# Optimization experiments

Measured on AMD Instinct MI355X. Metric: run time of the kernel, lower is better.

## Reference

```python
import math
import jax, jax.numpy as jnp
import numpy as np

B, F, NH, NB = 8, 400, 100, 65
SR, BLOCK = 16000, 128


def scale_function(x):
    # 2 * sigmoid(x)^log(10) + 1e-7 (standard ddsp_pytorch scale_function)
    return 2.0 * jax.nn.sigmoid(x) ** math.log(10.0) + 1e-7


def fft_convolve(signal, kernel):
    # signal: (..., L), kernel: (..., Lk); zero-pad, circular conv via rfft, keep 2nd half
    L = signal.shape[-1]
    Lk = kernel.shape[-1]
    s = jnp.pad(signal, [(0, 0)] * (signal.ndim - 1) + [(0, L)])
    k = jnp.pad(kernel, [(0, 0)] * (kernel.ndim - 1) + [(Lk, 0)])
    out = jnp.fft.irfft(jnp.fft.rfft(s) * jnp.fft.rfft(k))
    return out[..., out.shape[-1] // 2:]


def setup_inputs() -> dict:
    key = jax.random.key(0)
    k1, k2, k3, k4, k5 = jax.random.split(key, 5)
    return {
        "amp_param": jax.random.normal(k1, (B, F, NH + 1), jnp.float32),
        "noise_param": jax.random.normal(k2, (B, F, NB), jnp.float32),
        "pitch": jax.random.uniform(k3, (B, F, 1), jnp.float32) * 440.0 + 60.0,
        "noise": jax.random.uniform(k4, (B, F, BLOCK), jnp.float32) * 2.0 - 1.0,
        "reverb_noise": jax.random.uniform(k5, (SR, 1), jnp.float32) * 2.0 - 1.0,
        "decay": jnp.ones((1,), jnp.float32) * 5.0,
        "wet": jnp.zeros((1,), jnp.float32),
        "sampling_rate": SR,
        "block_size": BLOCK,
    }


def reference(amp_param, noise_param, pitch, noise, reverb_noise, decay, wet,
              sampling_rate, block_size):
    sr = float(sampling_rate)
    # ---- harmonic branch ----
    param = scale_function(amp_param)            # (B,F,NH+1)
    total_amp = param[..., :1]
    amps = param[..., 1:]                        # (B,F,NH)
    nh = amps.shape[-1]
    harm_idx = jnp.arange(1, nh + 1, dtype=amps.dtype)
    # remove_above_nyquist
    aa = (pitch * harm_idx < sr / 2).astype(amps.dtype) + 1e-4
    amps = amps * aa
    amps = amps / amps.sum(-1, keepdims=True)
    amps = amps * total_amp
    # nearest-neighbor upsample by block_size (torch interpolate default 'nearest')
    amps_up = jnp.repeat(amps, block_size, axis=1)    # (B,T,NH)
    pitch_up = jnp.repeat(pitch, block_size, axis=1)  # (B,T,1)
    # harmonic_synth: cumulative phase oscillator bank
    omega = jnp.cumsum(2.0 * math.pi * pitch_up / sr, axis=1)  # (B,T,1)
    harmonic = (jnp.sin(omega * harm_idx) * amps_up).sum(-1, keepdims=True)  # (B,T,1)

    # ---- filtered-noise branch ----
    nparam = scale_function(noise_param - 5.0)   # (B,F,NB)
    ir = jnp.fft.irfft(nparam.astype(jnp.complex64))  # (B,F,2*(NB-1))
    fs = ir.shape[-1]
    ir = jnp.roll(ir, fs // 2, axis=-1)
    win = 0.5 - 0.5 * jnp.cos(2.0 * math.pi * jnp.arange(fs, dtype=ir.dtype) / fs)
    ir = ir * win
    ir = jnp.pad(ir, ((0, 0), (0, 0), (0, block_size - fs)))
    ir = jnp.roll(ir, -(fs // 2), axis=-1)
    nz = fft_convolve(noise, ir)                 # (B,F,block)
    nz = nz.reshape(nz.shape[0], -1, 1)          # (B,T,1)

    signal = harmonic + nz                       # (B,T,1)

    # ---- reverb ----
    lenx = signal.shape[1]
    length = reverb_noise.shape[0]               # == sampling_rate
    t = (jnp.arange(length, dtype=signal.dtype) / sr).reshape(1, -1, 1)
    env = jnp.exp(-jax.nn.softplus(-decay[0]) * t * 500.0)
    impulse = reverb_noise * env * jax.nn.sigmoid(wet[0])   # (1,length,1)
    impulse = impulse.at[:, 0].set(1.0)
    impulse = jnp.pad(impulse, ((0, 0), (0, lenx - length), (0, 0)))
    out = fft_convolve(signal[..., 0], impulse[..., 0])[..., None]  # (B,T,1)
    return out
```

## Files before the change

### kernel.cpp

```cpp
#include <hip/hip_runtime.h>
#include <math.h>

#define NBATCH 8
#define NFRAME 400
#define NHARM  100
#define NBAND  65
#define SRATE  16000
#define BLK    128
#define NSAMP  (NFRAME*BLK)
#define PI_D   3.14159265358979323846

#define FFTN   4096
#define HOP    2048
#define NPART  8
#define NHOPS  (NSAMP / HOP)
#define NPAIR  (NBATCH / 2)
#define FTH    1024
#define NCONV  (NPAIR * NHOPS)

#define OFF_SIG    25600
#define OFF_H      1729536
#define OFF_X      1991680

typedef float2 cplx;

__device__ __forceinline__ int conv_swz(int bid) {
    int xcd = bid & 7, idx = bid >> 3;
    int base = (xcd < 4) ? xcd * 13 : 52 + (xcd - 4) * 12;
    return base + idx;
}

__device__ __forceinline__ cplx cmul(cplx a, cplx b) {
    return make_float2(a.x * b.x - a.y * b.y, a.x * b.y + a.y * b.x);
}
template <int SIGN>
__device__ __forceinline__ cplx rot90(cplx z) {
    return (SIGN < 0) ? make_float2(z.y, -z.x) : make_float2(-z.y, z.x);
}

template <int SIGN>
__device__ __forceinline__ void fft_dif_4096(cplx* A, int tid) {
    #pragma unroll
    for (int t = 12; t >= 2; t -= 2) {
        const int Q = 1 << (t - 2), h = 1 << (t - 1);
        __syncthreads();
        {
            int g = tid;
            int j = g & (Q - 1);
            int a = ((g >> (t - 2)) << t) + j;
            cplx x0 = A[a], x1 = A[a + Q], x2 = A[a + h], x3 = A[a + h + Q];
            float ang = (float)(2.0 * PI_D) * (float)j / (float)(1 << t);
            float sn, cs; __sincosf(ang, &sn, &cs);
            cplx w1 = make_float2(cs, (float)SIGN * sn);
            cplx w3 = make_float2(cs * cs - sn * sn, 2.0f * cs * sn * (float)SIGN);
            cplx p0 = make_float2(x0.x + x2.x, x0.y + x2.y);
            cplx p2 = cmul(make_float2(x0.x - x2.x, x0.y - x2.y), w1);
            cplx p1 = make_float2(x1.x + x3.x, x1.y + x3.y);
            cplx p3 = rot90<SIGN>(cmul(make_float2(x1.x - x3.x, x1.y - x3.y), w1));
            A[a]         = make_float2(p0.x + p1.x, p0.y + p1.y);
            A[a + Q]     = cmul(make_float2(p0.x - p1.x, p0.y - p1.y), w3);
            A[a + h]     = make_float2(p2.x + p3.x, p2.y + p3.y);
            A[a + h + Q] = cmul(make_float2(p2.x - p3.x, p2.y - p3.y), w3);
        }
    }
    __syncthreads();
}

template <int SIGN>
__device__ __forceinline__ void fft_dit_4096(cplx* A, int tid) {
    #pragma unroll
    for (int t = 2; t <= 12; t += 2) {
        const int Q = 1 << (t - 2), h = 1 << (t - 1);
        __syncthreads();
        {
            int g = tid;
            int j = g & (Q - 1);
            int a = ((g >> (t - 2)) << t) + j;
            cplx x0 = A[a], x1 = A[a + Q], x2 = A[a + h], x3 = A[a + h + Q];
            float ang = (float)(2.0 * PI_D) * (float)j / (float)(1 << t);
            float sn, cs; __sincosf(ang, &sn, &cs);
            cplx w1 = make_float2(cs, (float)SIGN * sn);
            cplx w3 = make_float2(cs * cs - sn * sn, 2.0f * cs * sn * (float)SIGN);
            cplx b1 = cmul(x1, w3);
            cplx q0 = make_float2(x0.x + b1.x, x0.y + b1.y);
            cplx q1 = make_float2(x0.x - b1.x, x0.y - b1.y);
            cplx b3 = cmul(x3, w3);
            cplx q2 = make_float2(x2.x + b3.x, x2.y + b3.y);
            cplx q3 = make_float2(x2.x - b3.x, x2.y - b3.y);
            cplx c2 = cmul(q2, w1);
            cplx c3 = rot90<SIGN>(cmul(q3, w1));
            A[a]         = make_float2(q0.x + c2.x, q0.y + c2.y);
            A[a + h]     = make_float2(q0.x - c2.x, q0.y - c2.y);
            A[a + Q]     = make_float2(q1.x + c3.x, q1.y + c3.y);
            A[a + h + Q] = make_float2(q1.x - c3.x, q1.y - c3.y);
        }
    }
    __syncthreads();
}

__device__ __forceinline__ float scale_fn(float x) {
    float s = 1.0f / (1.0f + __expf(-x));
    return 2.0f * __expf(2.3025851f * __logf(s)) + 1e-7f;
}

__global__ __launch_bounds__(128) void k_synth(const float* __restrict__ amp_param,
                                               const float* __restrict__ noise_param,
                                               const float* __restrict__ pitch,
                                               const float* __restrict__ noise,
                                               float* __restrict__ sig) {
    __shared__ float s_famps[NHARM];
    __shared__ float s_np[NBAND];
    __shared__ float s_ir[BLK];
    __shared__ float s_noise[BLK];
    __shared__ float s_red[BLK];
    __shared__ double s_dsum[2];
    __shared__ float s_fsum[2];
    __shared__ float s_total;

    int bf = blockIdx.x;
    int tid = threadIdx.x;
    int b  = bf / NFRAME, f0 = bf % NFRAME;
    float pf = pitch[bf];

    double ps = 0.0;
    {
        const float* prow = pitch + b * NFRAME;
        for (int j = tid; j < f0; j += BLK) ps += (double)prow[j];
    }

    float myamp = 0.0f;
    if (tid < NHARM + 1) {
        float p = scale_fn(amp_param[bf * (NHARM + 1) + tid]);
        if (tid == 0) s_total = p;
        else {
            float aa = (pf * (float)tid < 8000.0f) ? 1.0001f : 0.0001f;
            myamp = p * aa;
        }
    }
    if (tid < NBAND) s_np[tid] = scale_fn(noise_param[bf * NBAND + tid] - 5.0f);
    s_noise[tid] = noise[bf * BLK + tid];

    double rp = ps; float ra = myamp;
    #pragma unroll
    for (int off = 32; off >= 1; off >>= 1) {
        rp += __shfl_xor(rp, off);
        ra += __shfl_xor(ra, off);
    }
    if ((tid & 63) == 0) { s_dsum[tid >> 6] = rp; s_fsum[tid >> 6] = ra; }
    __syncthreads();

    double prefix_b = s_dsum[0] + s_dsum[1];
    float red = s_fsum[0] + s_fsum[1];
    if (tid >= 1 && tid <= NHARM) s_famps[tid - 1] = myamp / red * s_total;

    float irv;
    {
        float ang = (float)(2.0 * PI_D / 128.0) * (float)tid;
        float sn, c; __sincosf(ang, &sn, &c);
        float tcc = 2.0f * c;
        float u1 = c;
        float u2 = fmaf(tcc, u1, -1.0f);
        float u3 = fmaf(tcc, u2, -u1);
        float u4 = fmaf(tcc, u3, -u2);
        float u5 = fmaf(tcc, u4, -u3);
        float u6 = fmaf(tcc, u5, -u4);
        float u7 = fmaf(tcc, u6, -u5);
        float t0 = s_np[4] * u4;
        float t1 = fmaf(s_np[5], u5, s_np[1] * u1);
        float t2 = fmaf(s_np[6], u6, s_np[2] * u2);
        float t3 = fmaf(s_np[7], u7, s_np[3] * u3);
        float cc4  = fmaf(2.0f * u2, u2, -1.0f);
        float tc4a = 2.0f * cc4;
        float A0 = 1.0f, A1 = u1, A2 = u2, A3 = u3;
        float B0 = u4,   B1 = u5, B2 = u6, B3 = u7;
        #pragma unroll
        for (int g = 0; g < 14; ++g) {
            float n0 = fmaf(tc4a, B0, -A0); t0 = fmaf(s_np[8 + 4 * g + 0], n0, t0); A0 = B0; B0 = n0;
            float n1 = fmaf(tc4a, B1, -A1); t1 = fmaf(s_np[8 + 4 * g + 1], n1, t1); A1 = B1; B1 = n1;
            float n2 = fmaf(tc4a, B2, -A2); t2 = fmaf(s_np[8 + 4 * g + 2], n2, t2); A2 = B2; B2 = n2;
            float n3 = fmaf(tc4a, B3, -A3); t3 = fmaf(s_np[8 + 4 * g + 3], n3, t3); A3 = B3; B3 = n3;
        }
        float u64 = fmaf(tc4a, B0, -A0);
        float tt = (t0 + t1) + (t2 + t3);
        float a = fmaf(2.0f, tt, s_np[0]);
        a = fmaf(s_np[64], u64, a);
        a *= (1.0f / 128.0f);
        a *= fmaf(0.5f, c, 0.5f);
        irv = a;
    }
    s_ir[tid] = irv;
    __syncthreads();

    float accA = 0.0f;
    {
        int p1 = tid, h1 = (p1 + 2) >> 1;
        int m = 0;
        for (; m + 1 < h1; m += 2) {
            float i0 = s_ir[p1 - m], i1 = s_ir[p1 - m - 1];
            accA = fmaf(s_noise[m], i0, accA);
            accA = fmaf(s_noise[m + 1], i1, accA);
        }
        if (m < h1) accA = fmaf(s_noise[m], s_ir[p1 - m], accA);
    }
    {
        int p2 = 127 - tid, h2 = (p2 + 2) >> 1;
        float accB = 0.0f;
        int m = h2;
        for (; m + 1 <= p2; m += 2) {
            float i0 = s_ir[p2 - m], i1 = s_ir[p2 - m - 1];
            accB = fmaf(s_noise[m], i0, accB);
            accB = fmaf(s_noise[m + 1], i1, accB);
        }
        if (m <= p2) accB = fmaf(s_noise[m], s_ir[p2 - m], accB);
        s_red[p2] = accB;
    }
    __syncthreads();
    float nzv = accA + s_red[tid];

    double q = (128.0 * prefix_b + (double)(tid + 1) * (double)pf) * (1.0 / 16000.0);
    float th = (float)(q - floor(q)) * (float)(2.0 * PI_D);
    float h;
    {
        float s1v, c1v; __sincosf(th, &s1v, &c1v);
        float tc = 2.0f * c1v;
        float sk0 = s1v;
        float sk1 = tc * s1v;
        float sk2 = fmaf(tc, sk1, -sk0);
        float sk3 = fmaf(tc, sk2, -sk1);
        float sk4 = fmaf(tc, sk3, -sk2);
        float sk5 = fmaf(tc, sk4, -sk3);
        float sk6 = fmaf(tc, sk5, -sk4);
        float sk7 = fmaf(tc, sk6, -sk5);
        float h0 = fmaf(sk4, s_famps[4], sk0 * s_famps[0]);
        float h1 = fmaf(sk5, s_famps[5], sk1 * s_famps[1]);
        float h2 = fmaf(sk6, s_famps[6], sk2 * s_famps[2]);
        float h3 = fmaf(sk7, s_famps[7], sk3 * s_famps[3]);
        float cs2 = fmaf(tc, c1v, -1.0f);
        float cs4 = fmaf(2.0f * cs2, cs2, -1.0f);
        float tc4 = 2.0f * cs4;
        float a0 = sk0, a1 = sk1, a2 = sk2, a3 = sk3;
        float b0 = sk4, b1 = sk5, b2 = sk6, b3 = sk7;
        #pragma unroll
        for (int g = 0; g < 23; ++g) {
            float n0 = fmaf(tc4, b0, -a0); h0 = fmaf(n0, s_famps[8 + 4 * g + 0], h0); a0 = b0; b0 = n0;
            float n1 = fmaf(tc4, b1, -a1); h1 = fmaf(n1, s_famps[8 + 4 * g + 1], h1); a1 = b1; b1 = n1;
            float n2 = fmaf(tc4, b2, -a2); h2 = fmaf(n2, s_famps[8 + 4 * g + 2], h2); a2 = b2; b2 = n2;
            float n3 = fmaf(tc4, b3, -a3); h3 = fmaf(n3, s_famps[8 + 4 * g + 3], h3); a3 = b3; b3 = n3;
        }
        h = (h0 + h1) + (h2 + h3);
    }
    sig[bf * BLK + tid] = h + nzv;
}

__global__ __launch_bounds__(FTH) void k_fftsig(const float* __restrict__ sig,
                                                const float* __restrict__ rn,
                                                const float* __restrict__ decay,
                                                const float* __restrict__ wet,
                                                cplx* __restrict__ X,
                                                cplx* __restrict__ H) {
    __shared__ cplx sA[FFTN];
    int bid = blockIdx.x;
    int tid = threadIdx.x;

    if (bid >= NCONV) {
        int p = bid - NCONV;
        double c  = log1p(exp(-(double)decay[0])) * (500.0 / (double)SRATE);
        double wg = 1.0 / (1.0 + exp(-(double)wet[0]));
        for (int i = tid; i < FFTN; i += FTH) {
            float v = 0.0f;
            if (i < HOP) {
                int t = p * HOP + i;
                if (t == 0)         v = 1.0f;
                else if (t < SRATE) v = rn[t] * (float)(exp(-c * (double)t) * wg);
            }
            sA[i] = make_float2(v, 0.0f);
        }
        fft_dif_4096<-1>(sA, tid);
        const float s = 1.0f / (float)FFTN;
        for (int i = tid; i < FFTN; i += FTH) {
            cplx v = sA[i];
            H[p * FFTN + i] = make_float2(v.x * s, v.y * s);
        }
        return;
    }

    int bm = conv_swz(bid);
    int pb = bm / NHOPS, m = bm % NHOPS;
    const float* sa = sig + (2 * pb) * NSAMP;
    const float* sb = sa + NSAMP;
    int base = HOP * (m - 1);
    for (int i = tid; i < FFTN; i += FTH) {
        int idx = base + i;
        float va = 0.0f, vb = 0.0f;
        if (idx >= 0) { va = sa[idx]; vb = sb[idx]; }
        sA[i] = make_float2(va, vb);
    }
    fft_dif_4096<-1>(sA, tid);
    for (int i = tid; i < FFTN; i += FTH) X[bm * FFTN + i] = sA[i];
}

__global__ __launch_bounds__(FTH) void k_specmac_ifft(const cplx* __restrict__ X,
                                                      const cplx* __restrict__ H,
                                                      float* __restrict__ out) {
    __shared__ cplx sA[FFTN];
    int bm = conv_swz(blockIdx.x);
    int pb = bm / NHOPS, m = bm % NHOPS;
    int tid = threadIdx.x;

    cplx acc[4];
    #pragma unroll
    for (int it = 0; it < 4; ++it) acc[it] = make_float2(0.0f, 0.0f);

    int pmax = (m < NPART - 1) ? m : (NPART - 1);
    for (int p = 0; p <= pmax; ++p) {
        const cplx* Xm = X + (pb * NHOPS + (m - p)) * FFTN;
        const cplx* Hp = H + p * FFTN;
        #pragma unroll
        for (int it = 0; it < 4; ++it) {
            int i = tid + (it << 10);
            cplx xv = Xm[i], hv = Hp[i];
            cplx pr = cmul(xv, hv);
            acc[it].x += pr.x; acc[it].y += pr.y;
        }
    }
    #pragma unroll
    for (int it = 0; it < 4; ++it) sA[tid + (it << 10)] = acc[it];

    fft_dit_4096<1>(sA, tid);

    float* ob0 = out + (2 * pb) * NSAMP + m * HOP;
    float* ob1 = ob0 + NSAMP;
    #pragma unroll
    for (int it = 0; it < 2; ++it) {
        int j = tid + (it << 10);
        cplx v = sA[HOP + j];
        ob0[j] = v.x;
        ob1[j] = v.y;
    }
}

extern "C" void kernel_launch(void* const* d_in, const int* in_sizes, int n_in,
                              void* d_out, int out_size, void* d_ws, size_t ws_size,
                              hipStream_t stream) {
    const float* amp_param   = (const float*)d_in[0];
    const float* noise_param = (const float*)d_in[1];
    const float* pitch       = (const float*)d_in[2];
    const float* noise       = (const float*)d_in[3];
    const float* rn          = (const float*)d_in[4];
    const float* decay       = (const float*)d_in[5];
    const float* wet         = (const float*)d_in[6];
    float* out = (float*)d_out;

    char* ws = (char*)d_ws;
    float*  sig    = (float*)(ws + OFF_SIG);
    cplx*   H      = (cplx*)(ws + OFF_H);
    cplx*   X      = (cplx*)(ws + OFF_X);

    k_synth<<<dim3(NBATCH * NFRAME), dim3(128), 0, stream>>>(amp_param, noise_param, pitch, noise, sig);
    k_fftsig<<<dim3(NCONV + NPART), dim3(FTH), 0, stream>>>(sig, rn, decay, wet, X, H);
    k_specmac_ifft<<<dim3(NCONV), dim3(FTH), 0, stream>>>(X, H, out);
}
```

Before: 37.50 us.

## Switch 4096-point FFTs from radix-4 to radix-8 with 512 threads

Replaces the six-pass radix-4 DIF/DIT shared-memory FFTs with four-pass radix-8 versions using an inline 8-point DFT and twiddles built from one sincos. Block size drops from 1024 to 512 threads, so each thread handles 8 elements in the spectral MAC and output loops. The aim is fewer LDS round trips and barriers per FFT, at the cost of more registers per thread and extra twiddle multiplies that may add rounding error.

New measurement: 36.04 us. -3.9%, faster.

```diff
diff --git a/kernel.cpp b/kernel.cpp
--- a/kernel.cpp
+++ b/kernel.cpp
@@ -9,13 +9,14 @@
 #define BLK    128
 #define NSAMP  (NFRAME*BLK)
 #define PI_D   3.14159265358979323846
+#define C8     0.70710678118654752f
 
 #define FFTN   4096
 #define HOP    2048
 #define NPART  8
 #define NHOPS  (NSAMP / HOP)
 #define NPAIR  (NBATCH / 2)
-#define FTH    1024
+#define FTH    512
 #define NCONV  (NPAIR * NHOPS)
 
 #define OFF_SIG    25600
@@ -33,67 +34,101 @@
 __device__ __forceinline__ cplx cmul(cplx a, cplx b) {
     return make_float2(a.x * b.x - a.y * b.y, a.x * b.y + a.y * b.x);
 }
+__device__ __forceinline__ cplx cadd(cplx a, cplx b) { return make_float2(a.x + b.x, a.y + b.y); }
+__device__ __forceinline__ cplx csub(cplx a, cplx b) { return make_float2(a.x - b.x, a.y - b.y); }
 template <int SIGN>
 __device__ __forceinline__ cplx rot90(cplx z) {
     return (SIGN < 0) ? make_float2(z.y, -z.x) : make_float2(-z.y, z.x);
 }
-
-template <int SIGN>
-__device__ __forceinline__ void fft_dif_4096(cplx* A, int tid) {
-    #pragma unroll
-    for (int t = 12; t >= 2; t -= 2) {
-        const int Q = 1 << (t - 2), h = 1 << (t - 1);
+template <int SIGN>
+__device__ __forceinline__ cplx mul_w8(cplx z) {
+    return (SIGN < 0) ? make_float2(C8 * (z.x + z.y), C8 * (z.y - z.x))
+                      : make_float2(C8 * (z.x - z.y), C8 * (z.y + z.x));
+}
+
+template <int SIGN>
+__device__ __forceinline__ void dft8(cplx v[8]) {
+    cplx s0 = cadd(v[0], v[4]), s1 = cadd(v[1], v[5]);
+    cplx s2 = cadd(v[2], v[6]), s3 = cadd(v[3], v[7]);
+    cplx d0 = csub(v[0], v[4]), d1 = csub(v[1], v[5]);
+    cplx d2 = csub(v[2], v[6]), d3 = csub(v[3], v[7]);
+    cplx t0 = cadd(s0, s2), t1 = csub(s0, s2), t2 = cadd(s1, s3), t3 = csub(s1, s3);
+    cplx E0 = cadd(t0, t2), E2 = csub(t0, t2);
+    cplx r3 = rot90<SIGN>(t3);
+    cplx E1 = cadd(t1, r3), E3 = csub(t1, r3);
+    cplx o1 = mul_w8<SIGN>(d1);
+    cplx o2 = rot90<SIGN>(d2);
+    cplx o3 = rot90<SIGN>(mul_w8<SIGN>(d3));
+    cplx u0 = cadd(d0, o2), u1 = csub(d0, o2), u2 = cadd(o1, o3), u3 = csub(o1, o3);
+    cplx O0 = cadd(u0, u2), O2 = csub(u0, u2);
+    cplx r7 = rot90<SIGN>(u3);
+    cplx O1 = cadd(u1, r7), O3 = csub(u1, r7);
+    v[0] = E0; v[2] = E1; v[4] = E2; v[6] = E3;
+    v[1] = O0; v[3] = O1; v[5] = O2; v[7] = O3;
+}
+
+template <int SIGN>
+__device__ __forceinline__ void fft8_dif(cplx* A, int tid) {
+    #pragma unroll
+    for (int t = 12; t >= 3; t -= 3) {
+        const int Q = 1 << (t - 3);
         __syncthreads();
-        {
-            int g = tid;
-            int j = g & (Q - 1);
-            int a = ((g >> (t - 2)) << t) + j;
-            cplx x0 = A[a], x1 = A[a + Q], x2 = A[a + h], x3 = A[a + h + Q];
-            float ang = (float)(2.0 * PI_D) * (float)j / (float)(1 << t);
-            float sn, cs; __sincosf(ang, &sn, &cs);
-            cplx w1 = make_float2(cs, (float)SIGN * sn);
-            cplx w3 = make_float2(cs * cs - sn * sn, 2.0f * cs * sn * (float)SIGN);
-            cplx p0 = make_float2(x0.x + x2.x, x0.y + x2.y);
-            cplx p2 = cmul(make_float2(x0.x - x2.x, x0.y - x2.y), w1);
-            cplx p1 = make_float2(x1.x + x3.x, x1.y + x3.y);
-            cplx p3 = rot90<SIGN>(cmul(make_float2(x1.x - x3.x, x1.y - x3.y), w1));
-            A[a]         = make_float2(p0.x + p1.x, p0.y + p1.y);
-            A[a + Q]     = cmul(make_float2(p0.x - p1.x, p0.y - p1.y), w3);
-            A[a + h]     = make_float2(p2.x + p3.x, p2.y + p3.y);
-            A[a + h + Q] = cmul(make_float2(p2.x - p3.x, p2.y - p3.y), w3);
-        }
-    }
-    __syncthreads();
-}
-
-template <int SIGN>
-__device__ __forceinline__ void fft_dit_4096(cplx* A, int tid) {
-    #pragma unroll
-    for (int t = 2; t <= 12; t += 2) {
-        const int Q = 1 << (t - 2), h = 1 << (t - 1);
+        int j = tid & (Q - 1);
+        int a = ((tid >> (t - 3)) << t) + j;
+        cplx v[8];
+        #pragma unroll
+        for (int k = 0; k < 8; ++k) v[k] = A[a + k * Q];
+        dft8<SIGN>(v);
+        float ang = (float)(2.0 * PI_D) * (float)j / (float)(1 << t);
+        float sn, cs; __sincosf(ang, &sn, &cs);
+        cplx w1 = make_float2(cs, (float)SIGN * sn);
+        cplx w2 = cmul(w1, w1);
+        cplx w3 = cmul(w2, w1);
+        cplx w4 = cmul(w2, w2);
+        cplx w5 = cmul(w4, w1);
+        cplx w6 = cmul(w4, w2);
+        cplx w7 = cmul(w4, w3);
+        A[a]         = v[0];
+        A[a + Q]     = cmul(v[1], w1);
+        A[a + 2 * Q] = cmul(v[2], w2);
+        A[a + 3 * Q] = cmul(v[3], w3);
+        A[a + 4 * Q] = cmul(v[4], w4);
+        A[a + 5 * Q] = cmul(v[5], w5);
+        A[a + 6 * Q] = cmul(v[6], w6);
+        A[a + 7 * Q] = cmul(v[7], w7);
+    }
+    __syncthreads();
+}
+
+template <int SIGN>
+__device__ __forceinline__ void fft8_dit(cplx* A, int tid) {
+    #pragma unroll
+    for (int t = 3; t <= 12; t += 3) {
+        const int Q = 1 << (t - 3);
         __syncthreads();
-        {
-            int g = tid;
-            int j = g & (Q - 1);
-            int a = ((g >> (t - 2)) << t) + j;
-            cplx x0 = A[a], x1 = A[a + Q], x2 = A[a + h], x3 = A[a + h + Q];
-            float ang = (float)(2.0 * PI_D) * (float)j / (float)(1 << t);
-            float sn, cs; __sincosf(ang, &sn, &cs);
-            cplx w1 = make_float2(cs, (float)SIGN * sn);
-            cplx w3 = make_float2(cs * cs - sn * sn, 2.0f * cs * sn * (float)SIGN);
-            cplx b1 = cmul(x1, w3);
-            cplx q0 = make_float2(x0.x + b1.x, x0.y + b1.y);
-            cplx q1 = make_float2(x0.x - b1.x, x0.y - b1.y);
-            cplx b3 = cmul(x3, w3);
-            cplx q2 = make_float2(x2.x + b3.x, x2.y + b3.y);
-            cplx q3 = make_float2(x2.x - b3.x, x2.y - b3.y);
-            cplx c2 = cmul(q2, w1);
-            cplx c3 = rot90<SIGN>(cmul(q3, w1));
-            A[a]         = make_float2(q0.x + c2.x, q0.y + c2.y);
-            A[a + h]     = make_float2(q0.x - c2.x, q0.y - c2.y);
-            A[a + Q]     = make_float2(q1.x + c3.x, q1.y + c3.y);
-            A[a + h + Q] = make_float2(q1.x - c3.x, q1.y - c3.y);
-        }
+        int j = tid & (Q - 1);
+        int a = ((tid >> (t - 3)) << t) + j;
+        float ang = (float)(2.0 * PI_D) * (float)j / (float)(1 << t);
+        float sn, cs; __sincosf(ang, &sn, &cs);
+        cplx w1 = make_float2(cs, (float)SIGN * sn);
+        cplx w2 = cmul(w1, w1);
+        cplx w3 = cmul(w2, w1);
+        cplx w4 = cmul(w2, w2);
+        cplx w5 = cmul(w4, w1);
+        cplx w6 = cmul(w4, w2);
+        cplx w7 = cmul(w4, w3);
+        cplx v[8];
+        v[0] = A[a];
+        v[1] = cmul(A[a + Q], w1);
+        v[2] = cmul(A[a + 2 * Q], w2);
+        v[3] = cmul(A[a + 3 * Q], w3);
+        v[4] = cmul(A[a + 4 * Q], w4);
+        v[5] = cmul(A[a + 5 * Q], w5);
+        v[6] = cmul(A[a + 6 * Q], w6);
+        v[7] = cmul(A[a + 7 * Q], w7);
+        dft8<SIGN>(v);
+        #pragma unroll
+        for (int k = 0; k < 8; ++k) A[a + k * Q] = v[k];
     }
     __syncthreads();
 }
@@ -275,7 +310,7 @@
             }
             sA[i] = make_float2(v, 0.0f);
         }
-        fft_dif_4096<-1>(sA, tid);
+        fft8_dif<-1>(sA, tid);
         const float s = 1.0f / (float)FFTN;
         for (int i = tid; i < FFTN; i += FTH) {
             cplx v = sA[i];
@@ -295,7 +330,7 @@
         if (idx >= 0) { va = sa[idx]; vb = sb[idx]; }
         sA[i] = make_float2(va, vb);
     }
-    fft_dif_4096<-1>(sA, tid);
+    fft8_dif<-1>(sA, tid);
     for (int i = tid; i < FFTN; i += FTH) X[bm * FFTN + i] = sA[i];
 }
 
@@ -307,32 +342,32 @@
     int pb = bm / NHOPS, m = bm % NHOPS;
     int tid = threadIdx.x;
 
-    cplx acc[4];
-    #pragma unroll
-    for (int it = 0; it < 4; ++it) acc[it] = make_float2(0.0f, 0.0f);
+    cplx acc[8];
+    #pragma unroll
+    for (int it = 0; it < 8; ++it) acc[it] = make_float2(0.0f, 0.0f);
 
     int pmax = (m < NPART - 1) ? m : (NPART - 1);
     for (int p = 0; p <= pmax; ++p) {
         const cplx* Xm = X + (pb * NHOPS + (m - p)) * FFTN;
         const cplx* Hp = H + p * FFTN;
         #pragma unroll
-        for (int it = 0; it < 4; ++it) {
-            int i = tid + (it << 10);
+        for (int it = 0; it < 8; ++it) {
+            int i = tid + (it << 9);
             cplx xv = Xm[i], hv = Hp[i];
             cplx pr = cmul(xv, hv);
             acc[it].x += pr.x; acc[it].y += pr.y;
         }
     }
     #pragma unroll
-    for (int it = 0; it < 4; ++it) sA[tid + (it << 10)] = acc[it];
-
-    fft_dit_4096<1>(sA, tid);
+    for (int it = 0; it < 8; ++it) sA[tid + (it << 9)] = acc[it];
+
+    fft8_dit<1>(sA, tid);
 
     float* ob0 = out + (2 * pb) * NSAMP + m * HOP;
     float* ob1 = ob0 + NSAMP;
     #pragma unroll
-    for (int it = 0; it < 2; ++it) {
-        int j = tid + (it << 10);
+    for (int it = 0; it < 4; ++it) {
+        int j = tid + (it << 9);
         cplx v = sA[HOP + j];
         ob0[j] = v.x;
         ob1[j] = v.y;
```
